# Performance work log

Hardware: AMD Instinct MI355X
Metric: run time of the kernel (lower is better)

The kernel has to match this reference:

```python
import jax, jax.numpy as jnp
import numpy as np

EMBED = 768
HIDDEN = 3072
HEADS = 12
EPS = 1e-6


def _ln(x, g, b):
    mu = jnp.mean(x, axis=-1, keepdims=True)
    var = jnp.mean(jnp.square(x - mu), axis=-1, keepdims=True)
    return (x - mu) / jnp.sqrt(var + EPS) * g + b


def setup_inputs() -> dict:
    key = jax.random.key(0)
    ks = jax.random.split(key, 12)
    s = lambda fan_in: 1.0 / np.sqrt(fan_in)
    x = jax.random.normal(ks[0], (16, 1024, EMBED), dtype=jnp.float32)
    return {
        "x": x,
        "ln1_g": jnp.ones((EMBED,), jnp.float32),
        "ln1_b": jnp.zeros((EMBED,), jnp.float32),
        "qkv_w": jax.random.uniform(ks[1], (3 * EMBED, EMBED), jnp.float32, -s(EMBED), s(EMBED)),
        "qkv_b": jax.random.uniform(ks[2], (3 * EMBED,), jnp.float32, -s(EMBED), s(EMBED)),
        "proj_w": jax.random.uniform(ks[3], (EMBED, EMBED), jnp.float32, -s(EMBED), s(EMBED)),
        "proj_b": jax.random.uniform(ks[4], (EMBED,), jnp.float32, -s(EMBED), s(EMBED)),
        "ln2_g": jnp.ones((EMBED,), jnp.float32),
        "ln2_b": jnp.zeros((EMBED,), jnp.float32),
        "fc1_w": jax.random.uniform(ks[5], (HIDDEN, EMBED), jnp.float32, -s(EMBED), s(EMBED)),
        "fc1_b": jax.random.uniform(ks[6], (HIDDEN,), jnp.float32, -s(EMBED), s(EMBED)),
        "fc2_w": jax.random.uniform(ks[7], (EMBED, HIDDEN), jnp.float32, -s(HIDDEN), s(HIDDEN)),
        "fc2_b": jax.random.uniform(ks[8], (EMBED,), jnp.float32, -s(HIDDEN), s(HIDDEN)),
    }


def reference(x, ln1_g, ln1_b, qkv_w, qkv_b, proj_w, proj_b, ln2_g, ln2_b, fc1_w, fc1_b, fc2_w, fc2_b):
    B, N, D = x.shape
    Hd = D // HEADS
    scale = Hd ** -0.5
    # attention branch
    xn = _ln(x, ln1_g, ln1_b)
    qkv = xn @ qkv_w.T + qkv_b  # [B,N,3D]
    qkv = qkv.reshape(B, N, 3, HEADS, Hd).transpose(2, 0, 3, 1, 4)
    q, k, v = qkv[0], qkv[1], qkv[2]  # [B,H,N,Hd]
    attn = jax.nn.softmax(jnp.einsum("bhqd,bhkd->bhqk", q, k) * scale, axis=-1)
    ctx = jnp.einsum("bhqk,bhkd->bhqd", attn, v)
    ctx = ctx.transpose(0, 2, 1, 3).reshape(B, N, D)
    x = x + ctx @ proj_w.T + proj_b
    # MLP branch
    h = _ln(x, ln2_g, ln2_b)
    h = jax.nn.gelu(h @ fc1_w.T + fc1_b, approximate=False)
    x = x + h @ fc2_w.T + fc2_b
    return x
```

## Files before the change

### kernel.cpp

```cpp
#include <hip/hip_runtime.h>
#include <math.h>


typedef unsigned short u16;
typedef __attribute__((ext_vector_type(8))) short bf16x8;
typedef __attribute__((ext_vector_type(4))) float f32x4;

#define MFMA_BF16(a, b, c) __builtin_amdgcn_mfma_f32_16x16x32_bf16((a), (b), (c), 0, 0, 0)
#define MEMFENCE asm volatile("" ::: "memory")
#define WAITV(N) asm volatile("s_waitcnt vmcnt(" #N ")" ::: "memory")

__device__ __forceinline__ float bf2f(u16 v) {
    return __uint_as_float(((unsigned)v) << 16);
}
__device__ __forceinline__ u16 f2bf(float f) {
    unsigned u = __float_as_uint(f);
    u += 0x7fffu + ((u >> 16) & 1u);
    return (u16)(u >> 16);
}

__device__ __forceinline__ float gelu_fast(float v) {
    const float t = v * v;
    const float z = v * (1.5957691216f + 0.0713548162f * t);
    const float e = __expf(-z);
    return v * __builtin_amdgcn_rcpf(1.0f + e);
}

typedef __attribute__((address_space(1))) const void gvoid;
typedef __attribute__((address_space(3))) void lvoid;
__device__ __forceinline__ void gll16(const void* g, void* l) {
    __builtin_amdgcn_global_load_lds((gvoid*)g, (lvoid*)l, 16, 0, 0);
}

__global__ __launch_bounds__(256) void cast32(const float* __restrict__ src,
                                              u16* __restrict__ dst, int n8) {
    const int i = blockIdx.x * 256 + threadIdx.x;
    if (i >= n8) return;
    const float4 a = ((const float4*)src)[2 * i];
    const float4 b = ((const float4*)src)[2 * i + 1];
    bf16x8 r;
    r[0] = (short)f2bf(a.x); r[1] = (short)f2bf(a.y);
    r[2] = (short)f2bf(a.z); r[3] = (short)f2bf(a.w);
    r[4] = (short)f2bf(b.x); r[5] = (short)f2bf(b.y);
    r[6] = (short)f2bf(b.z); r[7] = (short)f2bf(b.w);
    ((bf16x8*)dst)[i] = r;
}

__global__ __launch_bounds__(256) void ln_kernel(const float* __restrict__ x,
                                                 const float* __restrict__ g,
                                                 const float* __restrict__ b,
                                                 u16* __restrict__ out) {
    const int row = blockIdx.x;
    const int t = threadIdx.x;
    const float* xr = x + (size_t)row * 768;
    float v0 = xr[t], v1 = xr[t + 256], v2 = xr[t + 512];
    float s = v0 + v1 + v2;
    float sq = v0 * v0 + v1 * v1 + v2 * v2;
#pragma unroll
    for (int off = 32; off > 0; off >>= 1) {
        s += __shfl_down(s, off);
        sq += __shfl_down(sq, off);
    }
    __shared__ float red_s[4], red_sq[4], sh_mu, sh_rs;
    const int wave = t >> 6, lane = t & 63;
    if (lane == 0) { red_s[wave] = s; red_sq[wave] = sq; }
    __syncthreads();
    if (t == 0) {
        float S = red_s[0] + red_s[1] + red_s[2] + red_s[3];
        float SQ = red_sq[0] + red_sq[1] + red_sq[2] + red_sq[3];
        float mu = S * (1.0f / 768.0f);
        float var = SQ * (1.0f / 768.0f) - mu * mu;
        sh_mu = mu;
        sh_rs = 1.0f / sqrtf(fmaxf(var, 0.0f) + 1e-6f);
    }
    __syncthreads();
    const float mu = sh_mu, rs = sh_rs;
    u16* orow = out + (size_t)row * 768;
    orow[t]       = f2bf((v0 - mu) * rs * g[t]       + b[t]);
    orow[t + 256] = f2bf((v1 - mu) * rs * g[t + 256] + b[t + 256]);
    orow[t + 512] = f2bf((v2 - mu) * rs * g[t + 512] + b[t + 512]);
}

template <int EPI, int BF16B>
__global__ __launch_bounds__(256, 2) void gemm2(
        const u16* __restrict__ A, const void* __restrict__ Bv,
        const float* __restrict__ bias, const float* __restrict__ res,
        void* __restrict__ Cv, u16* __restrict__ vtb, int N, int K) {
    __shared__ __align__(16) u16 As[128 * 32];
    __shared__ __align__(16) u16 Bs[128 * 32];
    const int t = threadIdx.x;
    const int wave = t >> 6, lane = t & 63;
    const int quad = lane >> 4, mr = lane & 15;
    const int wm = wave >> 1, wn = wave & 1;
    const int m0 = blockIdx.y * 128;
    const int n0 = blockIdx.x * 128;

    f32x4 acc[4][4];
#pragma unroll
    for (int i = 0; i < 4; i++)
#pragma unroll
        for (int j = 0; j < 4; j++) acc[i][j] = (f32x4){0.f, 0.f, 0.f, 0.f};

    const int seg = wave * 2;
    const int drow = lane >> 2;
    const int dcol = (lane & 3) * 8;
    const int sr = t >> 2, skv = t & 3;

    for (int k0 = 0; k0 < K; k0 += 32) {
#pragma unroll
        for (int c = 0; c < 2; c++) {
            const int rowA = (seg + c) * 16 + drow;
            gll16(A + (size_t)(m0 + rowA) * K + k0 + dcol, &As[(seg + c) * 512]);
        }
        if (BF16B) {
            const u16* Bh = (const u16*)Bv;
#pragma unroll
            for (int c = 0; c < 2; c++) {
                const int rowB = (seg + c) * 16 + drow;
                gll16(Bh + (size_t)(n0 + rowB) * K + k0 + dcol, &Bs[(seg + c) * 512]);
            }
        } else {
            const float* Bf = (const float*)Bv;
#pragma unroll
            for (int half = 0; half < 2; half++) {
                const float* src = Bf + (size_t)(n0 + sr + half * 64) * K + k0 + skv * 8;
                const float4 a = *(const float4*)src;
                const float4 b2 = *(const float4*)(src + 4);
                bf16x8 r;
                r[0] = (short)f2bf(a.x);  r[1] = (short)f2bf(a.y);
                r[2] = (short)f2bf(a.z);  r[3] = (short)f2bf(a.w);
                r[4] = (short)f2bf(b2.x); r[5] = (short)f2bf(b2.y);
                r[6] = (short)f2bf(b2.z); r[7] = (short)f2bf(b2.w);
                *(bf16x8*)&Bs[(sr + half * 64) * 32 + skv * 8] = r;
            }
        }
        __syncthreads();
        bf16x8 af[4], bfr[4];
#pragma unroll
        for (int i = 0; i < 4; i++)
            af[i] = *(const bf16x8*)&As[(wm * 64 + i * 16 + mr) * 32 + quad * 8];
#pragma unroll
        for (int j = 0; j < 4; j++)
            bfr[j] = *(const bf16x8*)&Bs[(wn * 64 + j * 16 + mr) * 32 + quad * 8];
#pragma unroll
        for (int i = 0; i < 4; i++)
#pragma unroll
            for (int j = 0; j < 4; j++)
                acc[i][j] = MFMA_BF16(af[i], bfr[j], acc[i][j]);
        __syncthreads();
    }

#pragma unroll
    for (int i = 0; i < 4; i++) {
#pragma unroll
        for (int r = 0; r < 4; r++) {
            const int m = m0 + wm * 64 + i * 16 + quad * 4 + r;
#pragma unroll
            for (int j = 0; j < 4; j++) {
                const int n = n0 + wn * 64 + j * 16 + mr;
                float v = acc[i][j][r] + bias[n];
                if (EPI == 1) {
                    v = gelu_fast(v);
                    ((u16*)Cv)[(size_t)m * N + n] = f2bf(v);
                } else if (EPI == 2) {
                    v += res[(size_t)m * N + n];
                    ((float*)Cv)[(size_t)m * N + n] = v;
                } else {
                    if (n < 1536) {
                        const float vq = (n < 768) ? v * 0.125f : v;
                        ((u16*)Cv)[(size_t)m * 1536 + n] = f2bf(vq);
                    } else {
                        const int h = (n - 1536) >> 6, hd = (n - 1536) & 63;
                        const int bb = m >> 10, pos = m & 1023;
                        vtb[((size_t)(bb * 12 + h) * 64 + hd) * 1024 + pos] = f2bf(v);
                    }
                }
            }
        }
    }
}

#define AFRAG(T, ROW, KS) \
    (*(const bf16x8*)&(T)[(ROW)][(((((KS) << 2) | quad)) ^ ((ROW) & 7)) << 3])

template <int EPI>
__global__ __launch_bounds__(512, 2) void gemm8(
        const u16* __restrict__ A, const u16* __restrict__ Bw,
        const float* __restrict__ bias, const float* __restrict__ res,
        void* __restrict__ Cv, u16* __restrict__ vtb, int N, int K) {
    __shared__ __align__(16) u16 As[2][256][64];
    __shared__ __align__(16) u16 Bs[2][256][64];
    const int t = threadIdx.x;
    const int wave = t >> 6, lane = t & 63;
    const int quad = lane >> 4, mr = lane & 15;
    const int wm = wave >> 2, wn = wave & 3;
    const int gx = gridDim.x;
    const int nwg = gx * gridDim.y;
    int bid = blockIdx.y * gx + blockIdx.x;
    bid = (bid & 7) * (nwg >> 3) + (bid >> 3);
    const int m0 = (bid / gx) * 256, n0 = (bid % gx) * 256;
    const int NT = K >> 6;

    const int srow = wave * 8 + (lane >> 3);
    const int sgrp = ((lane & 7) ^ (lane >> 3)) * 8;

#define STAGE_A(BI, SLOT, KT)                                                   \
    gll16(A + (size_t)(m0 + (SLOT) * 64 + srow) * K + (KT) * 64 + sgrp,         \
          &As[BI][(SLOT) * 64 + wave * 8][0])
#define STAGE_B(BI, SLOT, KT)                                                   \
    gll16(Bw + (size_t)(n0 + (SLOT) * 64 + srow) * K + (KT) * 64 + sgrp,        \
          &Bs[BI][(SLOT) * 64 + wave * 8][0])

    STAGE_A(0, 0, 0); STAGE_A(0, 2, 0);
    STAGE_B(0, 0, 0); STAGE_B(0, 1, 0);
    STAGE_B(0, 2, 0); STAGE_B(0, 3, 0);
    STAGE_A(0, 1, 0); STAGE_A(0, 3, 0);
    if (NT > 1) { STAGE_A(1, 0, 1); STAGE_A(1, 2, 1); STAGE_B(1, 0, 1); STAGE_B(1, 1, 1); }

    f32x4 acc[8][4];
#pragma unroll
    for (int i = 0; i < 8; i++)
#pragma unroll
        for (int j = 0; j < 4; j++) acc[i][j] = (f32x4){0.f, 0.f, 0.f, 0.f};

    if (NT > 1) { WAITV(6); } else { WAITV(2); }
    __builtin_amdgcn_s_barrier();
    MEMFENCE;

    for (int kt = 0; kt < NT; ++kt) {
        const int bi = kt & 1;
        const u16(*Ab)[64] = As[bi];
        const u16(*Bb)[64] = Bs[bi];
        const bool st1 = (kt + 1 < NT);
        const bool st2 = (kt + 2 < NT);
        bf16x8 af[4], bfv[4];

#pragma unroll
        for (int i = 0; i < 4; i++) af[i] = AFRAG(Ab, wm * 128 + i * 16 + mr, 0);
#pragma unroll
        for (int j = 0; j < 4; j++) bfv[j] = AFRAG(Bb, wn * 64 + j * 16 + mr, 0);
        if (st1) { STAGE_B(bi ^ 1, 2, kt + 1); STAGE_B(bi ^ 1, 3, kt + 1); }
        MEMFENCE;
        __builtin_amdgcn_s_barrier();
        MEMFENCE;
        __builtin_amdgcn_s_setprio(1);
#pragma unroll
        for (int i = 0; i < 4; i++)
#pragma unroll
            for (int j = 0; j < 4; j++)
                acc[i][j] = MFMA_BF16(af[i], bfv[j], acc[i][j]);
        __builtin_amdgcn_s_setprio(0);
        if (st1) { WAITV(6); } else { WAITV(0); }
        MEMFENCE;
        __builtin_amdgcn_s_barrier();
        MEMFENCE;

#pragma unroll
        for (int i = 0; i < 4; i++) af[i] = AFRAG(Ab, wm * 128 + 64 + i * 16 + mr, 0);
        if (st1) { STAGE_A(bi ^ 1, 1, kt + 1); STAGE_A(bi ^ 1, 3, kt + 1); }
        MEMFENCE;
        __builtin_amdgcn_s_barrier();
        MEMFENCE;
        __builtin_amdgcn_s_setprio(1);
#pragma unroll
        for (int i = 0; i < 4; i++)
#pragma unroll
            for (int j = 0; j < 4; j++)
                acc[4 + i][j] = MFMA_BF16(af[i], bfv[j], acc[4 + i][j]);
        __builtin_amdgcn_s_setprio(0);
        MEMFENCE;
        __builtin_amdgcn_s_barrier();
        MEMFENCE;

#pragma unroll
        for (int i = 0; i < 4; i++) af[i] = AFRAG(Ab, wm * 128 + i * 16 + mr, 1);
#pragma unroll
        for (int j = 0; j < 4; j++) bfv[j] = AFRAG(Bb, wn * 64 + j * 16 + mr, 1);
        MEMFENCE;
        __builtin_amdgcn_s_barrier();
        MEMFENCE;
        __builtin_amdgcn_s_setprio(1);
#pragma unroll
        for (int i = 0; i < 4; i++)
#pragma unroll
            for (int j = 0; j < 4; j++)
                acc[i][j] = MFMA_BF16(af[i], bfv[j], acc[i][j]);
        __builtin_amdgcn_s_setprio(0);
        MEMFENCE;
        __builtin_amdgcn_s_barrier();
        MEMFENCE;

#pragma unroll
        for (int i = 0; i < 4; i++) af[i] = AFRAG(Ab, wm * 128 + 64 + i * 16 + mr, 1);
        if (st2) { STAGE_A(bi, 0, kt + 2); STAGE_A(bi, 2, kt + 2);
                   STAGE_B(bi, 0, kt + 2); STAGE_B(bi, 1, kt + 2); }
        MEMFENCE;
        __builtin_amdgcn_s_barrier();
        MEMFENCE;
        __builtin_amdgcn_s_setprio(1);
#pragma unroll
        for (int i = 0; i < 4; i++)
#pragma unroll
            for (int j = 0; j < 4; j++)
                acc[4 + i][j] = MFMA_BF16(af[i], bfv[j], acc[4 + i][j]);
        __builtin_amdgcn_s_setprio(0);
        if (st2) { WAITV(6); } else if (st1) { WAITV(2); }
        MEMFENCE;
        __builtin_amdgcn_s_barrier();
        MEMFENCE;
    }

#pragma unroll
    for (int i = 0; i < 8; i++) {
#pragma unroll
        for (int r = 0; r < 4; r++) {
            const int m = m0 + wm * 128 + i * 16 + quad * 4 + r;
#pragma unroll
            for (int j = 0; j < 4; j++) {
                const int n = n0 + wn * 64 + j * 16 + mr;
                float v = acc[i][j][r] + bias[n];
                if (EPI == 1) {
                    v = gelu_fast(v);
                    ((u16*)Cv)[(size_t)m * N + n] = f2bf(v);
                } else if (EPI == 2) {
                    v += res[(size_t)m * N + n];
                    ((float*)Cv)[(size_t)m * N + n] = v;
                } else {
                    if (n < 1536) {
                        const float vq = (n < 768) ? v * 0.125f : v;
                        ((u16*)Cv)[(size_t)m * 1536 + n] = f2bf(vq);
                    } else {
                        const int h = (n - 1536) >> 6, hd = (n - 1536) & 63;
                        const int bb = m >> 10, pos = m & 1023;
                        vtb[((size_t)(bb * 12 + h) * 64 + hd) * 1024 + pos] = f2bf(v);
                    }
                }
            }
        }
    }
#undef STAGE_A
#undef STAGE_B
}

__global__ __launch_bounds__(256) void attn2(const u16* __restrict__ qkkb,
                                             const u16* __restrict__ vtb,
                                             u16* __restrict__ ctx) {
    __shared__ __align__(16) u16 Ks[2][64][72];
    __shared__ __align__(16) u16 Vt[2][64][72];
    __shared__ __align__(16) u16 Ps[64][72];
    const int bh = blockIdx.y;
    const int b = bh / 12, h = bh % 12;
    const int q0 = blockIdx.x * 64;
    const int t = threadIdx.x;
    const int wave = t >> 6, lane = t & 63, quad = lane >> 4, mr = lane & 15;

    const u16* qrow = qkkb + (size_t)(b * 1024 + q0 + wave * 16 + mr) * 1536 + h * 64;
    const bf16x8 qf0 = *(const bf16x8*)(qrow + quad * 8);
    const bf16x8 qf1 = *(const bf16x8*)(qrow + 32 + quad * 8);

    const u16* kbase = qkkb + (size_t)b * 1024 * 1536 + 768 + h * 64;
    const u16* vbase = vtb + (size_t)bh * 64 * 1024;

    const int srow = t >> 3;
    const int sv = t & 7;

    f32x4 oacc[4];
#pragma unroll
    for (int j = 0; j < 4; j++) oacc[j] = (f32x4){0.f, 0.f, 0.f, 0.f};
    float lsum[4] = {0.f, 0.f, 0.f, 0.f};

    bf16x8 pk0, pk1, pv0, pv1;
    pk0 = *(const bf16x8*)(kbase + (size_t)(srow)      * 1536 + sv * 8);
    pk1 = *(const bf16x8*)(kbase + (size_t)(srow + 32) * 1536 + sv * 8);
    pv0 = *(const bf16x8*)(vbase + (size_t)(srow)      * 1024 + sv * 8);
    pv1 = *(const bf16x8*)(vbase + (size_t)(srow + 32) * 1024 + sv * 8);
    *(bf16x8*)&Ks[0][srow][sv * 8] = pk0;
    *(bf16x8*)&Ks[0][srow + 32][sv * 8] = pk1;
    *(bf16x8*)&Vt[0][srow][sv * 8] = pv0;
    *(bf16x8*)&Vt[0][srow + 32][sv * 8] = pv1;

    for (int kt = 0; kt < 16; ++kt) {
        __syncthreads();
        const int cur = kt & 1;
        if (kt < 15) {
            const size_t ko = (size_t)(kt + 1) * 64;
            pk0 = *(const bf16x8*)(kbase + (ko + srow)      * 1536 + sv * 8);
            pk1 = *(const bf16x8*)(kbase + (ko + srow + 32) * 1536 + sv * 8);
            pv0 = *(const bf16x8*)(vbase + (size_t)(srow)      * 1024 + ko + sv * 8);
            pv1 = *(const bf16x8*)(vbase + (size_t)(srow + 32) * 1024 + ko + sv * 8);
        }
        f32x4 sf[4];
#pragma unroll
        for (int j = 0; j < 4; j++) {
            const bf16x8 kf0 = *(const bf16x8*)&Ks[cur][j * 16 + mr][quad * 8];
            const bf16x8 kf1 = *(const bf16x8*)&Ks[cur][j * 16 + mr][32 + quad * 8];
            f32x4 s = (f32x4){0.f, 0.f, 0.f, 0.f};
            s = MFMA_BF16(qf0, kf0, s);
            s = MFMA_BF16(qf1, kf1, s);
            sf[j] = s;
        }
#pragma unroll
        for (int r = 0; r < 4; r++) {
            const float p0 = __expf(sf[0][r] - 8.0f);
            const float p1 = __expf(sf[1][r] - 8.0f);
            const float p2 = __expf(sf[2][r] - 8.0f);
            const float p3 = __expf(sf[3][r] - 8.0f);
            lsum[r] += (p0 + p1) + (p2 + p3);
            const int prow = wave * 16 + quad * 4 + r;
            Ps[prow][0 * 16 + mr] = f2bf(p0);
            Ps[prow][1 * 16 + mr] = f2bf(p1);
            Ps[prow][2 * 16 + mr] = f2bf(p2);
            Ps[prow][3 * 16 + mr] = f2bf(p3);
        }
        __asm__ __volatile__("s_waitcnt lgkmcnt(0)" ::: "memory");
#pragma unroll
        for (int st = 0; st < 2; st++) {
            const bf16x8 pf = *(const bf16x8*)&Ps[wave * 16 + mr][st * 32 + quad * 8];
#pragma unroll
            for (int j = 0; j < 4; j++) {
                const bf16x8 vf = *(const bf16x8*)&Vt[cur][j * 16 + mr][st * 32 + quad * 8];
                oacc[j] = MFMA_BF16(pf, vf, oacc[j]);
            }
        }
        if (kt < 15) {
            const int nxt = cur ^ 1;
            *(bf16x8*)&Ks[nxt][srow][sv * 8] = pk0;
            *(bf16x8*)&Ks[nxt][srow + 32][sv * 8] = pk1;
            *(bf16x8*)&Vt[nxt][srow][sv * 8] = pv0;
            *(bf16x8*)&Vt[nxt][srow + 32][sv * 8] = pv1;
        }
    }

#pragma unroll
    for (int r = 0; r < 4; r++) {
#pragma unroll
        for (int off = 1; off < 16; off <<= 1) lsum[r] += __shfl_xor(lsum[r], off);
        const float inv = 1.0f / lsum[r];
        u16* dst = ctx + (size_t)(b * 1024 + q0 + wave * 16 + quad * 4 + r) * 768 + h * 64;
#pragma unroll
        for (int j = 0; j < 4; j++) dst[j * 16 + mr] = f2bf(oacc[j][r] * inv);
    }
}

extern "C" void kernel_launch(void* const* d_in, const int* in_sizes, int n_in,
                              void* d_out, int out_size, void* d_ws, size_t ws_size,
                              hipStream_t stream) {
    const float* x      = (const float*)d_in[0];
    const float* ln1_g  = (const float*)d_in[1];
    const float* ln1_b  = (const float*)d_in[2];
    const float* qkv_w  = (const float*)d_in[3];
    const float* qkv_b  = (const float*)d_in[4];
    const float* proj_w = (const float*)d_in[5];
    const float* proj_b = (const float*)d_in[6];
    const float* ln2_g  = (const float*)d_in[7];
    const float* ln2_b  = (const float*)d_in[8];
    const float* fc1_w  = (const float*)d_in[9];
    const float* fc1_b  = (const float*)d_in[10];
    const float* fc2_w  = (const float*)d_in[11];
    const float* fc2_b  = (const float*)d_in[12];
    float* out = (float*)d_out;

    char* base = (char*)d_ws + 1024;
    u16* xn   = (u16*)base;
    u16* qkkb = (u16*)(base + 25165824);
    u16* vtb  = (u16*)(base + 75497472);
    u16* h1   = (u16*)(base + 25165824);
    u16* ctxb = xn;
    u16* hn   = xn;

    const size_t WOFF = 125830144ull;
    const bool big = ws_size >= 139985920ull;
    u16* wqkv  = (u16*)((char*)d_ws + WOFF);
    u16* wproj = (u16*)((char*)d_ws + WOFF + 3538944);
    u16* wfc1  = (u16*)((char*)d_ws + WOFF + 4718592);
    u16* wfc2  = (u16*)((char*)d_ws + WOFF + 9437184);

    if (big) {
        cast32<<<dim3(864),  dim3(256), 0, stream>>>(qkv_w,  wqkv,  221184);
        cast32<<<dim3(288),  dim3(256), 0, stream>>>(proj_w, wproj, 73728);
        cast32<<<dim3(1152), dim3(256), 0, stream>>>(fc1_w,  wfc1,  294912);
        cast32<<<dim3(1152), dim3(256), 0, stream>>>(fc2_w,  wfc2,  294912);
    }

    ln_kernel<<<dim3(16384), dim3(256), 0, stream>>>(x, ln1_g, ln1_b, xn);

    if (big)
        gemm8<3><<<dim3(9, 64), dim3(512), 0, stream>>>(
            xn, wqkv, qkv_b, nullptr, qkkb, vtb, 2304, 768);
    else
        gemm2<3, 0><<<dim3(18, 128), dim3(256), 0, stream>>>(
            xn, qkv_w, qkv_b, nullptr, qkkb, vtb, 2304, 768);

    attn2<<<dim3(16, 192), dim3(256), 0, stream>>>(qkkb, vtb, ctxb);

    if (big)
        gemm8<2><<<dim3(3, 64), dim3(512), 0, stream>>>(
            ctxb, wproj, proj_b, x, out, nullptr, 768, 768);
    else
        gemm2<2, 0><<<dim3(6, 128), dim3(256), 0, stream>>>(
            ctxb, proj_w, proj_b, x, out, nullptr, 768, 768);

    ln_kernel<<<dim3(16384), dim3(256), 0, stream>>>(out, ln2_g, ln2_b, hn);

    if (big)
        gemm8<1><<<dim3(12, 64), dim3(512), 0, stream>>>(
            hn, wfc1, fc1_b, nullptr, h1, nullptr, 3072, 768);
    else
        gemm2<1, 0><<<dim3(24, 128), dim3(256), 0, stream>>>(
            hn, fc1_w, fc1_b, nullptr, h1, nullptr, 3072, 768);

    if (big)
        gemm8<2><<<dim3(3, 64), dim3(512), 0, stream>>>(
            h1, wfc2, fc2_b, out, out, nullptr, 768, 3072);
    else
        gemm2<2, 0><<<dim3(6, 128), dim3(256), 0, stream>>>(
            h1, fc2_w, fc2_b, out, out, nullptr, 768, 3072);
}
```

Before: 613.9 us.

## Stage V-transpose epilogue through LDS and tighten GEMM scheduling barriers

For the QKV GEMM tiles that produce V, the epilogue now writes bf16 results into a swizzled LDS buffer and then emits coalesced 8-byte stores of the transposed V layout. Before, each element was written with a strided 2-byte scattered store. The main loop also replaces compiler memory fences with sched_barrier plus explicit lgkmcnt waits, and precomputes the A/B base pointers to cut address arithmetic. This adds two __syncthreads and reuses the operand LDS in the epilogue.

Result: faster. 573.8 us (-6.5%).

```diff
diff --git a/kernel.cpp b/kernel.cpp
--- a/kernel.cpp
+++ b/kernel.cpp
@@ -9,6 +9,8 @@
 #define MFMA_BF16(a, b, c) __builtin_amdgcn_mfma_f32_16x16x32_bf16((a), (b), (c), 0, 0, 0)
 #define MEMFENCE asm volatile("" ::: "memory")
 #define WAITV(N) asm volatile("s_waitcnt vmcnt(" #N ")" ::: "memory")
+#define WAITLGKM0 asm volatile("s_waitcnt lgkmcnt(0)" ::: "memory")
+#define SCHED0 __builtin_amdgcn_sched_barrier(0)
 
 __device__ __forceinline__ float bf2f(u16 v) {
     return __uint_as_float(((unsigned)v) << 16);
@@ -188,8 +190,9 @@
         const u16* __restrict__ A, const u16* __restrict__ Bw,
         const float* __restrict__ bias, const float* __restrict__ res,
         void* __restrict__ Cv, u16* __restrict__ vtb, int N, int K) {
-    __shared__ __align__(16) u16 As[2][256][64];
-    __shared__ __align__(16) u16 Bs[2][256][64];
+    __shared__ __align__(16) u16 SMEM[4][256][64];
+    u16(&As)[2][256][64] = *reinterpret_cast<u16(*)[2][256][64]>(&SMEM[0][0][0]);
+    u16(&Bs)[2][256][64] = *reinterpret_cast<u16(*)[2][256][64]>(&SMEM[2][0][0]);
     const int t = threadIdx.x;
     const int wave = t >> 6, lane = t & 63;
     const int quad = lane >> 4, mr = lane & 15;
@@ -204,12 +207,13 @@
     const int srow = wave * 8 + (lane >> 3);
     const int sgrp = ((lane & 7) ^ (lane >> 3)) * 8;
 
-#define STAGE_A(BI, SLOT, KT)                                                   \
-    gll16(A + (size_t)(m0 + (SLOT) * 64 + srow) * K + (KT) * 64 + sgrp,         \
-          &As[BI][(SLOT) * 64 + wave * 8][0])
-#define STAGE_B(BI, SLOT, KT)                                                   \
-    gll16(Bw + (size_t)(n0 + (SLOT) * 64 + srow) * K + (KT) * 64 + sgrp,        \
-          &Bs[BI][(SLOT) * 64 + wave * 8][0])
+    const u16* Abase = A + (size_t)(m0 + srow) * K + sgrp;
+    const u16* Bbase = Bw + (size_t)(n0 + srow) * K + sgrp;
+
+#define STAGE_A(BI, SLOT, KT) \
+    gll16(Abase + ((size_t)(SLOT) * 64) * K + (KT) * 64, &As[BI][(SLOT) * 64 + wave * 8][0])
+#define STAGE_B(BI, SLOT, KT) \
+    gll16(Bbase + ((size_t)(SLOT) * 64) * K + (KT) * 64, &Bs[BI][(SLOT) * 64 + wave * 8][0])
 
     STAGE_A(0, 0, 0); STAGE_A(0, 2, 0);
     STAGE_B(0, 0, 0); STAGE_B(0, 1, 0);
@@ -225,7 +229,7 @@
 
     if (NT > 1) { WAITV(6); } else { WAITV(2); }
     __builtin_amdgcn_s_barrier();
-    MEMFENCE;
+    SCHED0;
 
     for (int kt = 0; kt < NT; ++kt) {
         const int bi = kt & 1;
@@ -240,9 +244,10 @@
 #pragma unroll
         for (int j = 0; j < 4; j++) bfv[j] = AFRAG(Bb, wn * 64 + j * 16 + mr, 0);
         if (st1) { STAGE_B(bi ^ 1, 2, kt + 1); STAGE_B(bi ^ 1, 3, kt + 1); }
-        MEMFENCE;
-        __builtin_amdgcn_s_barrier();
-        MEMFENCE;
+        SCHED0;
+        __builtin_amdgcn_s_barrier();
+        WAITLGKM0;
+        SCHED0;
         __builtin_amdgcn_s_setprio(1);
 #pragma unroll
         for (int i = 0; i < 4; i++)
@@ -250,17 +255,18 @@
             for (int j = 0; j < 4; j++)
                 acc[i][j] = MFMA_BF16(af[i], bfv[j], acc[i][j]);
         __builtin_amdgcn_s_setprio(0);
+        SCHED0;
         if (st1) { WAITV(6); } else { WAITV(0); }
-        MEMFENCE;
-        __builtin_amdgcn_s_barrier();
-        MEMFENCE;
+        __builtin_amdgcn_s_barrier();
+        SCHED0;
 
 #pragma unroll
         for (int i = 0; i < 4; i++) af[i] = AFRAG(Ab, wm * 128 + 64 + i * 16 + mr, 0);
         if (st1) { STAGE_A(bi ^ 1, 1, kt + 1); STAGE_A(bi ^ 1, 3, kt + 1); }
-        MEMFENCE;
-        __builtin_amdgcn_s_barrier();
-        MEMFENCE;
+        SCHED0;
+        __builtin_amdgcn_s_barrier();
+        WAITLGKM0;
+        SCHED0;
         __builtin_amdgcn_s_setprio(1);
 #pragma unroll
         for (int i = 0; i < 4; i++)
@@ -268,17 +274,18 @@
             for (int j = 0; j < 4; j++)
                 acc[4 + i][j] = MFMA_BF16(af[i], bfv[j], acc[4 + i][j]);
         __builtin_amdgcn_s_setprio(0);
-        MEMFENCE;
-        __builtin_amdgcn_s_barrier();
-        MEMFENCE;
+        SCHED0;
+        __builtin_amdgcn_s_barrier();
+        SCHED0;
 
 #pragma unroll
         for (int i = 0; i < 4; i++) af[i] = AFRAG(Ab, wm * 128 + i * 16 + mr, 1);
 #pragma unroll
         for (int j = 0; j < 4; j++) bfv[j] = AFRAG(Bb, wn * 64 + j * 16 + mr, 1);
-        MEMFENCE;
-        __builtin_amdgcn_s_barrier();
-        MEMFENCE;
+        SCHED0;
+        __builtin_amdgcn_s_barrier();
+        WAITLGKM0;
+        SCHED0;
         __builtin_amdgcn_s_setprio(1);
 #pragma unroll
         for (int i = 0; i < 4; i++)
@@ -286,17 +293,18 @@
             for (int j = 0; j < 4; j++)
                 acc[i][j] = MFMA_BF16(af[i], bfv[j], acc[i][j]);
         __builtin_amdgcn_s_setprio(0);
-        MEMFENCE;
-        __builtin_amdgcn_s_barrier();
-        MEMFENCE;
+        SCHED0;
+        __builtin_amdgcn_s_barrier();
+        SCHED0;
 
 #pragma unroll
         for (int i = 0; i < 4; i++) af[i] = AFRAG(Ab, wm * 128 + 64 + i * 16 + mr, 1);
         if (st2) { STAGE_A(bi, 0, kt + 2); STAGE_A(bi, 2, kt + 2);
                    STAGE_B(bi, 0, kt + 2); STAGE_B(bi, 1, kt + 2); }
-        MEMFENCE;
-        __builtin_amdgcn_s_barrier();
-        MEMFENCE;
+        SCHED0;
+        __builtin_amdgcn_s_barrier();
+        WAITLGKM0;
+        SCHED0;
         __builtin_amdgcn_s_setprio(1);
 #pragma unroll
         for (int i = 0; i < 4; i++)
@@ -304,35 +312,63 @@
             for (int j = 0; j < 4; j++)
                 acc[4 + i][j] = MFMA_BF16(af[i], bfv[j], acc[4 + i][j]);
         __builtin_amdgcn_s_setprio(0);
+        SCHED0;
         if (st2) { WAITV(6); } else if (st1) { WAITV(2); }
-        MEMFENCE;
-        __builtin_amdgcn_s_barrier();
-        MEMFENCE;
-    }
-
-#pragma unroll
-    for (int i = 0; i < 8; i++) {
-#pragma unroll
-        for (int r = 0; r < 4; r++) {
-            const int m = m0 + wm * 128 + i * 16 + quad * 4 + r;
+        __builtin_amdgcn_s_barrier();
+        SCHED0;
+    }
+
+    if (EPI == 3 && n0 >= 1536) {
+        u16* Ls = &SMEM[0][0][0];
+        __syncthreads();
+#pragma unroll
+        for (int i = 0; i < 8; i++) {
+            const int mbase = wm * 128 + i * 16 + quad * 4;
+            const int mch = mbase >> 3, mlo = mbase & 7;
 #pragma unroll
             for (int j = 0; j < 4; j++) {
-                const int n = n0 + wn * 64 + j * 16 + mr;
-                float v = acc[i][j][r] + bias[n];
-                if (EPI == 1) {
-                    v = gelu_fast(v);
-                    ((u16*)Cv)[(size_t)m * N + n] = f2bf(v);
-                } else if (EPI == 2) {
-                    v += res[(size_t)m * N + n];
-                    ((float*)Cv)[(size_t)m * N + n] = v;
-                } else {
-                    if (n < 1536) {
+                const int nl = wn * 64 + j * 16 + mr;
+                float v0 = acc[i][j][0] + bias[n0 + nl];
+                float v1 = acc[i][j][1] + bias[n0 + nl];
+                float v2 = acc[i][j][2] + bias[n0 + nl];
+                float v3 = acc[i][j][3] + bias[n0 + nl];
+                ushort4 w;
+                w.x = f2bf(v0); w.y = f2bf(v1); w.z = f2bf(v2); w.w = f2bf(v3);
+                *(ushort4*)(Ls + nl * 256 + ((mch ^ (nl & 7)) << 3) + mlo) = w;
+            }
+        }
+        __syncthreads();
+        const int bb = m0 >> 10, pos0 = m0 & 1023;
+#pragma unroll
+        for (int it = 0; it < 32; it++) {
+            const int nl = it * 8 + wave;
+            const int h = (n0 - 1536 + nl) >> 6;
+            const int hd = nl & 63;
+            const int mch = (lane >> 1) ^ (nl & 7);
+            const ushort4 v =
+                *(const ushort4*)(Ls + nl * 256 + (mch << 3) + (lane & 1) * 4);
+            u16* dst = vtb + ((size_t)(bb * 12 + h) * 64 + hd) * 1024 + pos0 + lane * 4;
+            *(ushort4*)dst = v;
+        }
+    } else {
+#pragma unroll
+        for (int i = 0; i < 8; i++) {
+#pragma unroll
+            for (int r = 0; r < 4; r++) {
+                const int m = m0 + wm * 128 + i * 16 + quad * 4 + r;
+#pragma unroll
+                for (int j = 0; j < 4; j++) {
+                    const int n = n0 + wn * 64 + j * 16 + mr;
+                    float v = acc[i][j][r] + bias[n];
+                    if (EPI == 1) {
+                        v = gelu_fast(v);
+                        ((u16*)Cv)[(size_t)m * N + n] = f2bf(v);
+                    } else if (EPI == 2) {
+                        v += res[(size_t)m * N + n];
+                        ((float*)Cv)[(size_t)m * N + n] = v;
+                    } else {
                         const float vq = (n < 768) ? v * 0.125f : v;
                         ((u16*)Cv)[(size_t)m * 1536 + n] = f2bf(vq);
-                    } else {
-                        const int h = (n - 1536) >> 6, hd = (n - 1536) & 63;
-                        const int bb = m >> 10, pos = m & 1023;
-                        vtb[((size_t)(bb * 12 + h) * 64 + hd) * 1024 + pos] = f2bf(v);
                     }
                 }
             }
```
